# Kernel optimization log

Measured on AMD Instinct MI355X. Metric: run time of the kernel, lower is better.

The kernel has to match this reference:

```python
import jax, jax.numpy as jnp
import numpy as np

N = 262144
D = 512
H = 512
G = 1024


def setup_inputs() -> dict:
    key = jax.random.key(0)
    k1, k2, k3, k4 = jax.random.split(key, 4)
    embed = jax.random.normal(k1, (N, D), dtype=jnp.float32)
    batch_index = jnp.sort(jax.random.randint(k2, (N,), 0, G)).astype(jnp.int64)
    # nn.Linear weights: W_att [atten_hidden, embed_size], V_att [1, atten_hidden]
    W_att = jax.random.normal(k3, (H, D), dtype=jnp.float32) * (1.0 / np.sqrt(D))
    V_att = jax.random.normal(k4, (1, H), dtype=jnp.float32) * (1.0 / np.sqrt(H))
    return {"embed": embed, "batch_index": batch_index, "W_att": W_att, "V_att": V_att, "num_segments": G}


def reference(embed, batch_index, W_att, V_att, num_segments):
    # beta = V(tanh(W(embed))).squeeze(-1)  -> [N]
    beta = jnp.einsum('nh,oh->no', jnp.tanh(jnp.einsum('nd,hd->nh', embed, W_att)), V_att).squeeze(-1)
    # segment softmax (unnormalized exp, as in the original module)
    exp_beta = jnp.exp(beta)
    grouped_sum = jax.ops.segment_sum(exp_beta, batch_index, num_segments=num_segments)  # [G]
    alpha = exp_beta / grouped_sum[batch_index]  # [N]
    # scatter-weighted sum of node embeddings per graph -> [G, D]
    result = jax.ops.segment_sum(alpha[:, None] * embed, batch_index, num_segments=num_segments)
    return result
```

## Files before the change

### kernel.cpp

```cpp
#include <hip/hip_runtime.h>
#include <hip/hip_bf16.h>

#define D_DIM 512
#define H_DIM 512
#define G_SEG 1024
#define BM    64

typedef __attribute__((ext_vector_type(8))) short bf16x8;
typedef __attribute__((ext_vector_type(4))) float f32x4;
typedef unsigned int u32;
typedef unsigned short u16;

#define WS_S   0
#define WS_WB  8192

#define AS_BYTES  (BM * 1024)
#define BETA_OFF  AS_BYTES
#define EBS_OFF   (BETA_OFF + 8 * BM * 4)
#define SIDX_OFF  (EBS_OFF + BM * 4)
#define LDS_TOTAL (SIDX_OFF + BM * 4)

static __device__ __forceinline__ u16 f2bf(float f) {
    __hip_bfloat16 h = __float2bfloat16(f);
    return *(u16*)&h;
}
static __device__ __forceinline__ float bf2f(u16 u) {
    return __uint_as_float(((u32)u) << 16);
}
static __device__ __forceinline__ float fast_tanh(float x) {
    float e = exp2f(x * 2.885390081777927f);
    return 1.0f - 2.0f * __builtin_amdgcn_rcpf(e + 1.0f);
}

__global__ __launch_bounds__(256)
void cvt_w(const float* __restrict__ W, u16* __restrict__ Wb) {
    int t   = blockIdx.x * 256 + threadIdx.x;
    int lhi = t & 3;
    int c   = (t >> 2) & 511;
    int k32 = t >> 11;
    const float* src = W + (size_t)c * 512 + k32 * 32 + lhi * 8;
    float4 f0 = *(const float4*)(src);
    float4 f1 = *(const float4*)(src + 4);
    u16 h[8];
    h[0]=f2bf(f0.x); h[1]=f2bf(f0.y); h[2]=f2bf(f0.z); h[3]=f2bf(f0.w);
    h[4]=f2bf(f1.x); h[5]=f2bf(f1.y); h[6]=f2bf(f1.z); h[7]=f2bf(f1.w);
    *(uint4*)(Wb + (size_t)t * 8) = *(uint4*)h;
}

__global__ __launch_bounds__(512, 4)
void fused(const float* __restrict__ E, const int* __restrict__ BI,
           const u16* __restrict__ Wb, const float* __restrict__ V,
           float* __restrict__ out, float* __restrict__ S)
{
    extern __shared__ char smem[];
    const int tid = threadIdx.x;
    const int nodeBase = blockIdx.x * BM;
    const int l   = tid & 63;
    const int w   = tid >> 6;
    const int l15 = l & 15;
    const int lhi = l >> 4;

    const float* Eb = E + (size_t)nodeBase * 512;
    const int arow = tid >> 3;
    const int aj   = tid & 7;

    f32x4 acc[4][4];
#pragma unroll
    for (int m = 0; m < 4; ++m)
#pragma unroll
        for (int n = 0; n < 4; ++n) acc[m][n] = (f32x4){0.f, 0.f, 0.f, 0.f};

    const int bOffBase = ((w * 64 + l15) * 4 + lhi) * 16;

    float4 aload[2];
    {
        const float* p0 = Eb + (size_t)arow * 512 + aj * 8;
        aload[0] = *(const float4*)p0;
        aload[1] = *(const float4*)(p0 + 4);
    }

    for (int ks = 0; ks < 8; ++ks) {
        {
            u16 h[8];
            h[0]=f2bf(aload[0].x); h[1]=f2bf(aload[0].y); h[2]=f2bf(aload[0].z); h[3]=f2bf(aload[0].w);
            h[4]=f2bf(aload[1].x); h[5]=f2bf(aload[1].y); h[6]=f2bf(aload[1].z); h[7]=f2bf(aload[1].w);
            int byte0 = arow * 1024 + ((ks * 128 + aj * 16) ^ ((arow & 7) << 4));
            *(uint4*)(smem + byte0) = *(uint4*)h;
        }
        if (ks < 7) {
            const float* p0 = Eb + (size_t)arow * 512 + (ks + 1) * 64 + aj * 8;
            aload[0] = *(const float4*)p0;
            aload[1] = *(const float4*)(p0 + 4);
        }
        __syncthreads();

#pragma unroll 1
        for (int ksub = 0; ksub < 2; ++ksub) {
            const char* Wsub = (const char*)Wb + ((size_t)(ks * 2 + ksub) << 15);
            bf16x8 b[4];
#pragma unroll
            for (int n = 0; n < 4; ++n)
                b[n] = *(const bf16x8*)(Wsub + bOffBase + n * 1024);
            bf16x8 a[4];
            const int kbyte = ks * 128 + ksub * 64 + lhi * 16;
#pragma unroll
            for (int m = 0; m < 4; ++m) {
                int row = m * 16 + l15;
                a[m] = *(const bf16x8*)(smem + row * 1024 + (kbyte ^ ((row & 7) << 4)));
            }
#pragma unroll
            for (int m = 0; m < 4; ++m)
#pragma unroll
                for (int n = 0; n < 4; ++n)
                    acc[m][n] = __builtin_amdgcn_mfma_f32_16x16x32_bf16(a[m], b[n], acc[m][n], 0, 0, 0);
        }
    }

    float Vv[4];
#pragma unroll
    for (int n = 0; n < 4; ++n)
        Vv[n] = V[w * 64 + n * 16 + l15];

    float bsum[4][4];
#pragma unroll
    for (int m = 0; m < 4; ++m)
#pragma unroll
        for (int r = 0; r < 4; ++r) {
            float s = 0.f;
#pragma unroll
            for (int n = 0; n < 4; ++n)
                s += Vv[n] * fast_tanh(acc[m][n][r]);
            bsum[m][r] = s;
        }
#pragma unroll
    for (int off = 1; off <= 8; off <<= 1)
#pragma unroll
        for (int m = 0; m < 4; ++m)
#pragma unroll
            for (int r = 0; r < 4; ++r)
                bsum[m][r] += __shfl_xor(bsum[m][r], off, 64);

    float* betaP = (float*)(smem + BETA_OFF);
    if (l15 == 0) {
#pragma unroll
        for (int m = 0; m < 4; ++m)
#pragma unroll
            for (int r = 0; r < 4; ++r)
                betaP[w * BM + m * 16 + lhi * 4 + r] = bsum[m][r];
    }
    __syncthreads();

    float* ebs  = (float*)(smem + EBS_OFF);
    int*   sidx = (int*)(smem + SIDX_OFF);
    if (tid < BM) {
        float beta = 0.f;
#pragma unroll
        for (int j = 0; j < 8; ++j)
            beta += betaP[j * BM + tid];
        float eb = expf(beta);
        ebs[tid] = eb;
        int g = BI[nodeBase + tid];
        sidx[tid] = g;
        int g0 = __shfl(g, 0, 64);
        if (__all(g == g0)) {
            float s = eb;
#pragma unroll
            for (int off = 1; off <= 32; off <<= 1)
                s += __shfl_xor(s, off, 64);
            if (l == 0) atomicAdd(&S[g], s);
        } else {
            atomicAdd(&S[g], eb);
        }
    }
    __syncthreads();

    {
        const int c = tid;
        float a = 0.f;
        int gcur = sidx[0];
        for (int r = 0; r < BM; ++r) {
            int g = sidx[r];
            if (g != gcur) {
                atomicAdd(&out[(size_t)gcur * 512 + c], a);
                a = 0.f; gcur = g;
            }
            u16 v = *(const u16*)(smem + r * 1024 + ((2 * c) ^ ((r & 7) << 4)));
            a += ebs[r] * bf2f(v);
        }
        atomicAdd(&out[(size_t)gcur * 512 + c], a);
    }
}

__global__ __launch_bounds__(256)
void finalize_kernel(float* __restrict__ out, const float* __restrict__ S) {
    int idx = blockIdx.x * 256 + threadIdx.x;
    float s = S[idx >> 9];
    float v = out[idx];
    out[idx] = (s != 0.f) ? v * __builtin_amdgcn_rcpf(s) : 0.f;
}

extern "C" void kernel_launch(void* const* d_in, const int* in_sizes, int n_in,
                              void* d_out, int out_size, void* d_ws, size_t ws_size,
                              hipStream_t stream) {
    const float* E  = (const float*)d_in[0];
    const int*   BI = (const int*)d_in[1];
    const float* W  = (const float*)d_in[2];
    const float* V  = (const float*)d_in[3];
    float* out = (float*)d_out;
    char*  ws  = (char*)d_ws;
    const int Ntot = in_sizes[0] / D_DIM;

    float* S  = (float*)(ws + WS_S);
    u16*   Wb = (u16*)(ws + WS_WB);

    hipMemsetAsync(S, 0, G_SEG * 4, stream);
    hipMemsetAsync(out, 0, (size_t)out_size * 4, stream);
    hipFuncSetAttribute((const void*)fused,
                        hipFuncAttributeMaxDynamicSharedMemorySize, LDS_TOTAL);

    cvt_w<<<128, 256, 0, stream>>>(W, Wb);
    fused<<<Ntot / BM, 512, LDS_TOTAL, stream>>>(E, BI, Wb, V, out, S);
    finalize_kernel<<<out_size / 256, 256, 0, stream>>>(out, S);
}
```

Measured before the change: 333.4 us.

## Load full embed tile into LDS upfront, then run MFMA loop with one barrier

The code now loads the whole 64x512 embed tile into LDS in two batched phases of eight float4 loads each, converting it to bf16 as it goes. One barrier follows, then all 16 k-steps of MFMA run without further synchronisation. Before, loads were software-pipelined one k-chunk at a time with a barrier per chunk. This puts more global loads in flight and drops seven barriers, but loses the overlap of global loads with MFMA work and raises register pressure.

New measurement: 367.5 us. 10.2% more time.

```diff
diff --git a/kernel.cpp b/kernel.cpp
--- a/kernel.cpp
+++ b/kernel.cpp
@@ -72,48 +72,52 @@
 
     const int bOffBase = ((w * 64 + l15) * 4 + lhi) * 16;
 
-    float4 aload[2];
     {
-        const float* p0 = Eb + (size_t)arow * 512 + aj * 8;
-        aload[0] = *(const float4*)p0;
-        aload[1] = *(const float4*)(p0 + 4);
-    }
-
-    for (int ks = 0; ks < 8; ++ks) {
-        {
-            u16 h[8];
-            h[0]=f2bf(aload[0].x); h[1]=f2bf(aload[0].y); h[2]=f2bf(aload[0].z); h[3]=f2bf(aload[0].w);
-            h[4]=f2bf(aload[1].x); h[5]=f2bf(aload[1].y); h[6]=f2bf(aload[1].z); h[7]=f2bf(aload[1].w);
-            int byte0 = arow * 1024 + ((ks * 128 + aj * 16) ^ ((arow & 7) << 4));
-            *(uint4*)(smem + byte0) = *(uint4*)h;
-        }
-        if (ks < 7) {
-            const float* p0 = Eb + (size_t)arow * 512 + (ks + 1) * 64 + aj * 8;
-            aload[0] = *(const float4*)p0;
-            aload[1] = *(const float4*)(p0 + 4);
-        }
-        __syncthreads();
-
+        const float* prow = Eb + (size_t)arow * 512 + aj * 8;
+        const int bytebase = arow * 1024;
+        const int swz = (arow & 7) << 4;
 #pragma unroll 1
-        for (int ksub = 0; ksub < 2; ++ksub) {
-            const char* Wsub = (const char*)Wb + ((size_t)(ks * 2 + ksub) << 15);
-            bf16x8 b[4];
+        for (int ph = 0; ph < 2; ++ph) {
+            float4 L[8];
+#pragma unroll
+            for (int q = 0; q < 4; ++q) {
+                const float* p = prow + (ph * 4 + q) * 64;
+                L[2 * q]     = *(const float4*)p;
+                L[2 * q + 1] = *(const float4*)(p + 4);
+            }
+#pragma unroll
+            for (int q = 0; q < 4; ++q) {
+                u16 h[8];
+                h[0]=f2bf(L[2*q].x);   h[1]=f2bf(L[2*q].y);
+                h[2]=f2bf(L[2*q].z);   h[3]=f2bf(L[2*q].w);
+                h[4]=f2bf(L[2*q+1].x); h[5]=f2bf(L[2*q+1].y);
+                h[6]=f2bf(L[2*q+1].z); h[7]=f2bf(L[2*q+1].w);
+                int byte0 = bytebase + (((ph * 4 + q) * 128 + aj * 16) ^ swz);
+                *(uint4*)(smem + byte0) = *(uint4*)h;
+            }
+        }
+    }
+    __syncthreads();
+
+#pragma unroll 1
+    for (int kk = 0; kk < 16; ++kk) {
+        const char* Wsub = (const char*)Wb + ((size_t)kk << 15);
+        bf16x8 b[4];
+#pragma unroll
+        for (int n = 0; n < 4; ++n)
+            b[n] = *(const bf16x8*)(Wsub + bOffBase + n * 1024);
+        bf16x8 a[4];
+        const int kbyte = kk * 64 + lhi * 16;
+#pragma unroll
+        for (int m = 0; m < 4; ++m) {
+            int row = m * 16 + l15;
+            a[m] = *(const bf16x8*)(smem + row * 1024 + (kbyte ^ ((row & 7) << 4)));
+        }
+#pragma unroll
+        for (int m = 0; m < 4; ++m)
 #pragma unroll
             for (int n = 0; n < 4; ++n)
-                b[n] = *(const bf16x8*)(Wsub + bOffBase + n * 1024);
-            bf16x8 a[4];
-            const int kbyte = ks * 128 + ksub * 64 + lhi * 16;
-#pragma unroll
-            for (int m = 0; m < 4; ++m) {
-                int row = m * 16 + l15;
-                a[m] = *(const bf16x8*)(smem + row * 1024 + (kbyte ^ ((row & 7) << 4)));
-            }
-#pragma unroll
-            for (int m = 0; m < 4; ++m)
-#pragma unroll
-                for (int n = 0; n < 4; ++n)
-                    acc[m][n] = __builtin_amdgcn_mfma_f32_16x16x32_bf16(a[m], b[n], acc[m][n], 0, 0, 0);
-        }
+                acc[m][n] = __builtin_amdgcn_mfma_f32_16x16x32_bf16(a[m], b[n], acc[m][n], 0, 0, 0);
     }
 
     float Vv[4];
```
